# Optimization experiments

Hardware: AMD Instinct MI355X
Metric: run time of the kernel (lower is better)

## Reference

```python
import jax, jax.numpy as jnp
import numpy as np

N, F_IN, F_OUT = 8192, 256, 128


def setup_inputs() -> dict:
    key = jax.random.key(0)
    k1, k2, k3, k4 = jax.random.split(key, 4)
    h = jax.random.normal(k1, (N, F_IN), dtype=jnp.float32)
    adj = jax.random.randint(k2, (N, N), 0, 2, dtype=jnp.int32)
    # xavier-uniform-like init scales
    w_lim = float(np.sqrt(6.0 / (F_IN + F_OUT)))
    a_lim = float(np.sqrt(6.0 / (2 * F_OUT + 1)))
    W = jax.random.uniform(k3, (F_IN, F_OUT), jnp.float32, -w_lim, w_lim)
    a = jax.random.uniform(k4, (2 * F_OUT, 1), jnp.float32, -a_lim, a_lim)
    return {"h": h, "adj": adj, "W": W, "a": a}


def reference(h, adj, W, a):
    # Wh: [N, F_OUT]
    Wh = h @ W
    # Fused form of the pairwise-concat score: e[i,j] = leakyrelu(Wh_i.a1 + Wh_j.a2)
    a1 = a[:F_OUT]   # [F_OUT, 1]
    a2 = a[F_OUT:]   # [F_OUT, 1]
    s1 = Wh @ a1     # [N, 1]
    s2 = Wh @ a2     # [N, 1]
    e = jax.nn.leaky_relu(s1 + s2.T, negative_slope=0.2)  # [N, N]
    e = jnp.where(adj > 0, e, jnp.float32(-9e15))
    attention = jax.nn.softmax(e, axis=1)
    return attention @ Wh  # [N, F_OUT]
```

## Files before the change

kernel.cpp:

```cpp
#include <hip/hip_runtime.h>

#define N_   8192
#define FIN  256
#define FOUT 128

typedef _Float16 f16x8 __attribute__((ext_vector_type(8)));
typedef _Float16 f16x4 __attribute__((ext_vector_type(4)));
typedef float    f32x4 __attribute__((ext_vector_type(4)));

__global__ __launch_bounds__(256) void k_wh(
    const float* __restrict__ h, const float* __restrict__ W,
    const float* __restrict__ a, float* __restrict__ Wh,
    float* __restrict__ s1, float* __restrict__ s2)
{
    __shared__ float hrow[2][FIN];
    __shared__ float rbuf[2][2][2];
    const int t   = threadIdx.x;
    const int rh  = t >> 7;
    const int c   = t & 127;
    const int row = (blockIdx.x << 1) + rh;

    hrow[rh][c]       = h[(size_t)row * FIN + c];
    hrow[rh][c + 128] = h[(size_t)row * FIN + c + 128];
    __syncthreads();

    float acc = 0.f;
    #pragma unroll 8
    for (int k = 0; k < FIN; ++k)
        acc = fmaf(hrow[rh][k], W[k * FOUT + c], acc);

    Wh[(size_t)row * FOUT + c] = acc;

    float p1 = acc * a[c];
    float p2 = acc * a[FOUT + c];
    #pragma unroll
    for (int off = 32; off; off >>= 1) {
        p1 += __shfl_down(p1, off, 64);
        p2 += __shfl_down(p2, off, 64);
    }
    if ((t & 63) == 0) { rbuf[rh][c >> 6][0] = p1; rbuf[rh][c >> 6][1] = p2; }
    __syncthreads();
    if (c == 0) {
        s1[row] = rbuf[rh][0][0] + rbuf[rh][1][0];
        s2[row] = rbuf[rh][0][1] + rbuf[rh][1][1];
    }
}

__global__ __launch_bounds__(256) void k_tr(
    const float* __restrict__ Wh, _Float16* __restrict__ WhT)
{
    __shared__ float tile[64][129];
    const int t = threadIdx.x;
    const int rbase = blockIdx.x * 64;

    #pragma unroll
    for (int q = 0; q < 8; ++q) {
        int i4 = q * 256 + t;
        int r  = i4 >> 5;
        int c4 = (i4 & 31) * 4;
        *(float4*)&tile[r][c4] = *(const float4*)&Wh[(size_t)(rbase + r) * FOUT + c4];
    }
    __syncthreads();

    const int c = t >> 1, half = t & 1;
    _Float16 buf[32];
    #pragma unroll
    for (int r = 0; r < 32; ++r) buf[r] = (_Float16)tile[32 * half + r][c];
    #pragma unroll
    for (int q = 0; q < 4; ++q)
        *(f16x8*)&WhT[(size_t)c * N_ + rbase + 32 * half + 8 * q] = *(f16x8*)&buf[8 * q];
}

__global__ __launch_bounds__(512, 4) void k_attn(
    const int* __restrict__ adj, const _Float16* __restrict__ WhT,
    const float* __restrict__ s1g, const float* __restrict__ s2g,
    float* __restrict__ num_g, float* __restrict__ den_g)
{
    __shared__ _Float16 pA[32 * 64];

    const int t  = threadIdx.x;
    const int w  = t >> 6;
    const int l  = t & 63;

    const int rb    = blockIdx.x & 255;
    const int sp    = blockIdx.x >> 8;
    const int rbase = rb * 32;
    const int jbase = sp * 2048;
    const int NT    = 2048 / 64;

    const int r  = t >> 4;
    const int j0 = (t & 15) << 2;
    const float s1r = s1g[rbase + r];
    const int* __restrict__ adjrow = adj + (size_t)(rbase + r) * N_;

    const int ln15 = l & 15, lq = l >> 4;
    const _Float16* __restrict__ bptr =
        WhT + (size_t)(16 * w + ln15) * N_ + 8 * lq;
    const int a_row0 = ln15;
    const int a_row1 = 16 + ln15;
    const int a_sw0  = (a_row0 & 7) << 3;
    const int a_sw1  = (a_row1 & 7) << 3;

    f32x4 acc0 = {0.f, 0.f, 0.f, 0.f};
    f32x4 acc1 = {0.f, 0.f, 0.f, 0.f};
    float denp = 0.f;

    int4   av  = *(const int4*)(adjrow + jbase + j0);
    float4 s2v = *(const float4*)(s2g + jbase + j0);

    for (int tile = 0; tile < NT; ++tile) {
        const int jb = jbase + tile * 64;

        float e, p0, p1, p2, p3;
        e = s1r + s2v.x; e = e > 0.f ? e : 0.2f * e; p0 = av.x ? __expf(e - 4.f) : 0.f;
        e = s1r + s2v.y; e = e > 0.f ? e : 0.2f * e; p1 = av.y ? __expf(e - 4.f) : 0.f;
        e = s1r + s2v.z; e = e > 0.f ? e : 0.2f * e; p2 = av.z ? __expf(e - 4.f) : 0.f;
        e = s1r + s2v.w; e = e > 0.f ? e : 0.2f * e; p3 = av.w ? __expf(e - 4.f) : 0.f;
        _Float16 h0 = (_Float16)p0, h1 = (_Float16)p1,
                 h2 = (_Float16)p2, h3 = (_Float16)p3;
        denp += (float)h0 + (float)h1 + (float)h2 + (float)h3;
        f16x4 pv = {h0, h1, h2, h3};
        *(f16x4*)(pA + r * 64 + (j0 ^ ((r & 7) << 3))) = pv;

        __syncthreads();

        const int jn = (tile + 1 < NT) ? jb + 64 : jbase;
        int4   av_n  = *(const int4*)(adjrow + jn + j0);
        float4 s2v_n = *(const float4*)(s2g + jn + j0);

        f16x8 b0 = *(const f16x8*)(bptr + jb);
        f16x8 b1 = *(const f16x8*)(bptr + jb + 32);

        f16x8 a00 = *(const f16x8*)(pA + a_row0 * 64 + ((8 * lq)      ^ a_sw0));
        f16x8 a01 = *(const f16x8*)(pA + a_row0 * 64 + ((32 + 8 * lq) ^ a_sw0));
        f16x8 a10 = *(const f16x8*)(pA + a_row1 * 64 + ((8 * lq)      ^ a_sw1));
        f16x8 a11 = *(const f16x8*)(pA + a_row1 * 64 + ((32 + 8 * lq) ^ a_sw1));

        acc0 = __builtin_amdgcn_mfma_f32_16x16x32_f16(a00, b0, acc0, 0, 0, 0);
        acc0 = __builtin_amdgcn_mfma_f32_16x16x32_f16(a01, b1, acc0, 0, 0, 0);
        acc1 = __builtin_amdgcn_mfma_f32_16x16x32_f16(a10, b0, acc1, 0, 0, 0);
        acc1 = __builtin_amdgcn_mfma_f32_16x16x32_f16(a11, b1, acc1, 0, 0, 0);

        __syncthreads();
        av = av_n; s2v = s2v_n;
    }

    denp += __shfl_xor(denp, 1, 64);
    denp += __shfl_xor(denp, 2, 64);
    denp += __shfl_xor(denp, 4, 64);
    denp += __shfl_xor(denp, 8, 64);
    if ((t & 15) == 0)
        den_g[(size_t)sp * N_ + rbase + r] = denp;

    const int colg = 16 * w + ln15;
    const int rq   = lq * 4;
    #pragma unroll
    for (int q = 0; q < 4; ++q) {
        num_g[((size_t)sp * N_ + rbase + rq + q)      * FOUT + colg] = acc0[q];
        num_g[((size_t)sp * N_ + rbase + 16 + rq + q) * FOUT + colg] = acc1[q];
    }
}

__global__ __launch_bounds__(256) void k_norm(
    const float* __restrict__ num_g, const float* __restrict__ den_g,
    float* __restrict__ out)
{
    const int idx4 = blockIdx.x * 256 + threadIdx.x;
    const int i  = idx4 >> 5;
    const int c4 = (idx4 & 31) * 4;

    float4 s = {0.f, 0.f, 0.f, 0.f};
    float  d = 0.f;
    #pragma unroll
    for (int sp = 0; sp < 4; ++sp) {
        float4 v = *(const float4*)(num_g + ((size_t)sp * N_ + i) * FOUT + c4);
        s.x += v.x; s.y += v.y; s.z += v.z; s.w += v.w;
        d += den_g[(size_t)sp * N_ + i];
    }
    const float inv = 1.f / d;
    float4 o = {s.x * inv, s.y * inv, s.z * inv, s.w * inv};
    *(float4*)&out[(size_t)i * FOUT + c4] = o;
}

extern "C" void kernel_launch(void* const* d_in, const int* in_sizes, int n_in,
                              void* d_out, int out_size, void* d_ws, size_t ws_size,
                              hipStream_t stream) {
    const float* h   = (const float*)d_in[0];
    const int*   adj = (const int*)d_in[1];
    const float* W   = (const float*)d_in[2];
    const float* a   = (const float*)d_in[3];
    float* out = (float*)d_out;

    char* ws = (char*)d_ws;
    float*    Wh  = (float*)ws;
    _Float16* WhT = (_Float16*)(ws + (4u << 20));
    float*    s1  = (float*)(ws + (6u << 20));
    float*    s2  = (float*)(ws + (6u << 20) + 32768);
    float*    num = (float*)(ws + (7u << 20));
    float*    den = (float*)(ws + (23u << 20));

    k_wh  <<<N_ / 2, 256, 0, stream>>>(h, W, a, Wh, s1, s2);
    k_tr  <<<N_ / 64, 256, 0, stream>>>(Wh, WhT);
    k_attn<<<1024, 512, 0, stream>>>(adj, WhT, s1, s2, num, den);
    k_norm<<<1024, 256, 0, stream>>>(num, den, out);
}
```

Baseline: 145.4 us.

## Double-buffer attention P tile with 128-wide K steps and LDS-staged s2

```diff
diff --git a/kernel.cpp b/kernel.cpp
--- a/kernel.cpp
+++ b/kernel.cpp
@@ -76,7 +76,8 @@
     const float* __restrict__ s1g, const float* __restrict__ s2g,
     float* __restrict__ num_g, float* __restrict__ den_g)
 {
-    __shared__ _Float16 pA[32 * 64];
+    __shared__ _Float16 pA[2][32][136];
+    __shared__ float s2s[2048];
 
     const int t  = threadIdx.x;
     const int w  = t >> 6;
@@ -86,64 +87,89 @@
     const int sp    = blockIdx.x >> 8;
     const int rbase = rb * 32;
     const int jbase = sp * 2048;
-    const int NT    = 2048 / 64;
+
+    *(float4*)&s2s[t * 4] = *(const float4*)&s2g[jbase + t * 4];
 
     const int r  = t >> 4;
-    const int j0 = (t & 15) << 2;
+    const int j0 = (t & 15) << 3;
     const float s1r = s1g[rbase + r];
-    const int* __restrict__ adjrow = adj + (size_t)(rbase + r) * N_;
+    const int* __restrict__ arow = adj + (size_t)(rbase + r) * N_ + jbase;
 
     const int ln15 = l & 15, lq = l >> 4;
     const _Float16* __restrict__ bptr =
-        WhT + (size_t)(16 * w + ln15) * N_ + 8 * lq;
-    const int a_row0 = ln15;
-    const int a_row1 = 16 + ln15;
-    const int a_sw0  = (a_row0 & 7) << 3;
-    const int a_sw1  = (a_row1 & 7) << 3;
+        WhT + (size_t)(16 * w + ln15) * N_ + jbase + 8 * lq;
 
     f32x4 acc0 = {0.f, 0.f, 0.f, 0.f};
     f32x4 acc1 = {0.f, 0.f, 0.f, 0.f};
     float denp = 0.f;
 
-    int4   av  = *(const int4*)(adjrow + jbase + j0);
-    float4 s2v = *(const float4*)(s2g + jbase + j0);
-
-    for (int tile = 0; tile < NT; ++tile) {
-        const int jb = jbase + tile * 64;
-
-        float e, p0, p1, p2, p3;
-        e = s1r + s2v.x; e = e > 0.f ? e : 0.2f * e; p0 = av.x ? __expf(e - 4.f) : 0.f;
-        e = s1r + s2v.y; e = e > 0.f ? e : 0.2f * e; p1 = av.y ? __expf(e - 4.f) : 0.f;
-        e = s1r + s2v.z; e = e > 0.f ? e : 0.2f * e; p2 = av.z ? __expf(e - 4.f) : 0.f;
-        e = s1r + s2v.w; e = e > 0.f ? e : 0.2f * e; p3 = av.w ? __expf(e - 4.f) : 0.f;
-        _Float16 h0 = (_Float16)p0, h1 = (_Float16)p1,
-                 h2 = (_Float16)p2, h3 = (_Float16)p3;
-        denp += (float)h0 + (float)h1 + (float)h2 + (float)h3;
-        f16x4 pv = {h0, h1, h2, h3};
-        *(f16x4*)(pA + r * 64 + (j0 ^ ((r & 7) << 3))) = pv;
-
-        __syncthreads();
-
-        const int jn = (tile + 1 < NT) ? jb + 64 : jbase;
-        int4   av_n  = *(const int4*)(adjrow + jn + j0);
-        float4 s2v_n = *(const float4*)(s2g + jn + j0);
-
+    auto computeP = [&](const int4& aA, const int4& aB, int tile, int buf) {
+        const float* s2p = &s2s[tile * 128 + j0];
+        float4 sA = *(const float4*)(s2p);
+        float4 sB = *(const float4*)(s2p + 4);
+        float m, e;
+        f16x8 pv;
+        m = s1r + sA.x; e = fmaxf(m, 0.2f * m); pv[0] = (_Float16)(aA.x ? __expf(e - 4.f) : 0.f);
+        m = s1r + sA.y; e = fmaxf(m, 0.2f * m); pv[1] = (_Float16)(aA.y ? __expf(e - 4.f) : 0.f);
+        m = s1r + sA.z; e = fmaxf(m, 0.2f * m); pv[2] = (_Float16)(aA.z ? __expf(e - 4.f) : 0.f);
+        m = s1r + sA.w; e = fmaxf(m, 0.2f * m); pv[3] = (_Float16)(aA.w ? __expf(e - 4.f) : 0.f);
+        m = s1r + sB.x; e = fmaxf(m, 0.2f * m); pv[4] = (_Float16)(aB.x ? __expf(e - 4.f) : 0.f);
+        m = s1r + sB.y; e = fmaxf(m, 0.2f * m); pv[5] = (_Float16)(aB.y ? __expf(e - 4.f) : 0.f);
+        m = s1r + sB.z; e = fmaxf(m, 0.2f * m); pv[6] = (_Float16)(aB.z ? __expf(e - 4.f) : 0.f);
+        m = s1r + sB.w; e = fmaxf(m, 0.2f * m); pv[7] = (_Float16)(aB.w ? __expf(e - 4.f) : 0.f);
+        denp += (float)pv[0] + (float)pv[1] + (float)pv[2] + (float)pv[3]
+              + (float)pv[4] + (float)pv[5] + (float)pv[6] + (float)pv[7];
+        *(f16x8*)&pA[buf][r][j0] = pv;
+    };
+
+    auto mmaTile = [&](int buf, int jb) {
         f16x8 b0 = *(const f16x8*)(bptr + jb);
         f16x8 b1 = *(const f16x8*)(bptr + jb + 32);
-
-        f16x8 a00 = *(const f16x8*)(pA + a_row0 * 64 + ((8 * lq)      ^ a_sw0));
-        f16x8 a01 = *(const f16x8*)(pA + a_row0 * 64 + ((32 + 8 * lq) ^ a_sw0));
-        f16x8 a10 = *(const f16x8*)(pA + a_row1 * 64 + ((8 * lq)      ^ a_sw1));
-        f16x8 a11 = *(const f16x8*)(pA + a_row1 * 64 + ((32 + 8 * lq) ^ a_sw1));
-
-        acc0 = __builtin_amdgcn_mfma_f32_16x16x32_f16(a00, b0, acc0, 0, 0, 0);
-        acc0 = __builtin_amdgcn_mfma_f32_16x16x32_f16(a01, b1, acc0, 0, 0, 0);
-        acc1 = __builtin_amdgcn_mfma_f32_16x16x32_f16(a10, b0, acc1, 0, 0, 0);
-        acc1 = __builtin_amdgcn_mfma_f32_16x16x32_f16(a11, b1, acc1, 0, 0, 0);
-
-        __syncthreads();
-        av = av_n; s2v = s2v_n;
-    }
+        f16x8 b2 = *(const f16x8*)(bptr + jb + 64);
+        f16x8 b3 = *(const f16x8*)(bptr + jb + 96);
+        const _Float16* a0p = &pA[buf][ln15][8 * lq];
+        const _Float16* a1p = &pA[buf][16 + ln15][8 * lq];
+        acc0 = __builtin_amdgcn_mfma_f32_16x16x32_f16(*(const f16x8*)(a0p),      b0, acc0, 0, 0, 0);
+        acc1 = __builtin_amdgcn_mfma_f32_16x16x32_f16(*(const f16x8*)(a1p),      b0, acc1, 0, 0, 0);
+        acc0 = __builtin_amdgcn_mfma_f32_16x16x32_f16(*(const f16x8*)(a0p + 32), b1, acc0, 0, 0, 0);
+        acc1 = __builtin_amdgcn_mfma_f32_16x16x32_f16(*(const f16x8*)(a1p + 32), b1, acc1, 0, 0, 0);
+        acc0 = __builtin_amdgcn_mfma_f32_16x16x32_f16(*(const f16x8*)(a0p + 64), b2, acc0, 0, 0, 0);
+        acc1 = __builtin_amdgcn_mfma_f32_16x16x32_f16(*(const f16x8*)(a1p + 64), b2, acc1, 0, 0, 0);
+        acc0 = __builtin_amdgcn_mfma_f32_16x16x32_f16(*(const f16x8*)(a0p + 96), b3, acc0, 0, 0, 0);
+        acc1 = __builtin_amdgcn_mfma_f32_16x16x32_f16(*(const f16x8*)(a1p + 96), b3, acc1, 0, 0, 0);
+    };
+
+    int4 av0A = *(const int4*)(arow + j0);
+    int4 av0B = *(const int4*)(arow + j0 + 4);
+    int4 av1A = *(const int4*)(arow + 128 + j0);
+    int4 av1B = *(const int4*)(arow + 128 + j0 + 4);
+
+    __syncthreads();
+    computeP(av0A, av0B, 0, 0);
+    __syncthreads();
+
+    for (int tt = 0; tt < 14; tt += 2) {
+        {
+            const int tn = tt + 2;
+            av0A = *(const int4*)(arow + tn * 128 + j0);
+            av0B = *(const int4*)(arow + tn * 128 + j0 + 4);
+            mmaTile(0, tt * 128);
+            computeP(av1A, av1B, tt + 1, 1);
+            __syncthreads();
+        }
+        {
+            const int tn = tt + 3;
+            av1A = *(const int4*)(arow + tn * 128 + j0);
+            av1B = *(const int4*)(arow + tn * 128 + j0 + 4);
+            mmaTile(1, (tt + 1) * 128);
+            computeP(av0A, av0B, tt + 2, 0);
+            __syncthreads();
+        }
+    }
+    mmaTile(0, 14 * 128);
+    computeP(av1A, av1B, 15, 1);
+    __syncthreads();
+    mmaTile(1, 15 * 128);
 
     denp += __shfl_xor(denp, 1, 64);
     denp += __shfl_xor(denp, 2, 64);
```

Result: faster. 132.2 us (-9.0%).

## Restructure attention kernel to per-wave 16-row tiles with register-only MFMA pipeline

Applied to the files above, without the earlier changes.

```diff
diff --git a/kernel.cpp b/kernel.cpp
--- a/kernel.cpp
+++ b/kernel.cpp
@@ -5,8 +5,8 @@
 #define FOUT 128
 
 typedef _Float16 f16x8 __attribute__((ext_vector_type(8)));
-typedef _Float16 f16x4 __attribute__((ext_vector_type(4)));
 typedef float    f32x4 __attribute__((ext_vector_type(4)));
+typedef unsigned int uint;
 
 __global__ __launch_bounds__(256) void k_wh(
     const float* __restrict__ h, const float* __restrict__ W,
@@ -41,13 +41,14 @@
     if ((t & 63) == 0) { rbuf[rh][c >> 6][0] = p1; rbuf[rh][c >> 6][1] = p2; }
     __syncthreads();
     if (c == 0) {
-        s1[row] = rbuf[rh][0][0] + rbuf[rh][1][0];
-        s2[row] = rbuf[rh][0][1] + rbuf[rh][1][1];
+        const float k2 = 1.44269504088896f;
+        s1[row] = (rbuf[rh][0][0] + rbuf[rh][1][0]) * k2;
+        s2[row] = (rbuf[rh][0][1] + rbuf[rh][1][1]) * k2;
     }
 }
 
 __global__ __launch_bounds__(256) void k_tr(
-    const float* __restrict__ Wh, _Float16* __restrict__ WhT)
+    const float* __restrict__ Wh, _Float16* __restrict__ WhTt)
 {
     __shared__ float tile[64][129];
     const int t = threadIdx.x;
@@ -66,98 +67,112 @@
     _Float16 buf[32];
     #pragma unroll
     for (int r = 0; r < 32; ++r) buf[r] = (_Float16)tile[32 * half + r][c];
+    _Float16* dst = WhTt + (size_t)(rbase / 32 + half) * 4096 + c * 32;
     #pragma unroll
     for (int q = 0; q < 4; ++q)
-        *(f16x8*)&WhT[(size_t)c * N_ + rbase + 32 * half + 8 * q] = *(f16x8*)&buf[8 * q];
-}
-
-__global__ __launch_bounds__(512, 4) void k_attn(
-    const int* __restrict__ adj, const _Float16* __restrict__ WhT,
+        *(f16x8*)(dst + 8 * q) = *(f16x8*)&buf[8 * q];
+}
+
+__global__ __launch_bounds__(256) void k_attn(
+    const int* __restrict__ adj, const _Float16* __restrict__ WhTt,
     const float* __restrict__ s1g, const float* __restrict__ s2g,
     float* __restrict__ num_g, float* __restrict__ den_g)
 {
-    __shared__ _Float16 pA[32 * 64];
-
     const int t  = threadIdx.x;
     const int w  = t >> 6;
     const int l  = t & 63;
-
-    const int rb    = blockIdx.x & 255;
-    const int sp    = blockIdx.x >> 8;
-    const int rbase = rb * 32;
+    const int ln15 = l & 15, lq = l >> 4;
+
+    const int sp    = blockIdx.x >> 7;
+    const int rg    = (blockIdx.x & 127) * 4 + w;
+    const int rbase = rg * 16;
     const int jbase = sp * 2048;
-    const int NT    = 2048 / 64;
-
-    const int r  = t >> 4;
-    const int j0 = (t & 15) << 2;
-    const float s1r = s1g[rbase + r];
-    const int* __restrict__ adjrow = adj + (size_t)(rbase + r) * N_;
-
-    const int ln15 = l & 15, lq = l >> 4;
-    const _Float16* __restrict__ bptr =
-        WhT + (size_t)(16 * w + ln15) * N_ + 8 * lq;
-    const int a_row0 = ln15;
-    const int a_row1 = 16 + ln15;
-    const int a_sw0  = (a_row0 & 7) << 3;
-    const int a_sw1  = (a_row1 & 7) << 3;
-
-    f32x4 acc0 = {0.f, 0.f, 0.f, 0.f};
-    f32x4 acc1 = {0.f, 0.f, 0.f, 0.f};
+
+    const float s1r = s1g[rbase + ln15];
+    const int* __restrict__ arow =
+        adj + (size_t)(rbase + ln15) * N_ + jbase + 8 * lq;
+    const float* __restrict__ s2p = s2g + jbase + 8 * lq;
+    const _Float16* __restrict__ bp =
+        WhTt + (size_t)(jbase >> 5) * 4096 + ln15 * 32 + 8 * lq;
+
+    f32x4 acc[8];
+    #pragma unroll
+    for (int g = 0; g < 8; ++g) acc[g] = (f32x4){0.f, 0.f, 0.f, 0.f};
     float denp = 0.f;
 
-    int4   av  = *(const int4*)(adjrow + jbase + j0);
-    float4 s2v = *(const float4*)(s2g + jbase + j0);
-
-    for (int tile = 0; tile < NT; ++tile) {
-        const int jb = jbase + tile * 64;
-
-        float e, p0, p1, p2, p3;
-        e = s1r + s2v.x; e = e > 0.f ? e : 0.2f * e; p0 = av.x ? __expf(e - 4.f) : 0.f;
-        e = s1r + s2v.y; e = e > 0.f ? e : 0.2f * e; p1 = av.y ? __expf(e - 4.f) : 0.f;
-        e = s1r + s2v.z; e = e > 0.f ? e : 0.2f * e; p2 = av.z ? __expf(e - 4.f) : 0.f;
-        e = s1r + s2v.w; e = e > 0.f ? e : 0.2f * e; p3 = av.w ? __expf(e - 4.f) : 0.f;
-        _Float16 h0 = (_Float16)p0, h1 = (_Float16)p1,
-                 h2 = (_Float16)p2, h3 = (_Float16)p3;
-        denp += (float)h0 + (float)h1 + (float)h2 + (float)h3;
-        f16x4 pv = {h0, h1, h2, h3};
-        *(f16x4*)(pA + r * 64 + (j0 ^ ((r & 7) << 3))) = pv;
-
-        __syncthreads();
-
-        const int jn = (tile + 1 < NT) ? jb + 64 : jbase;
-        int4   av_n  = *(const int4*)(adjrow + jn + j0);
-        float4 s2v_n = *(const float4*)(s2g + jn + j0);
-
-        f16x8 b0 = *(const f16x8*)(bptr + jb);
-        f16x8 b1 = *(const f16x8*)(bptr + jb + 32);
-
-        f16x8 a00 = *(const f16x8*)(pA + a_row0 * 64 + ((8 * lq)      ^ a_sw0));
-        f16x8 a01 = *(const f16x8*)(pA + a_row0 * 64 + ((32 + 8 * lq) ^ a_sw0));
-        f16x8 a10 = *(const f16x8*)(pA + a_row1 * 64 + ((8 * lq)      ^ a_sw1));
-        f16x8 a11 = *(const f16x8*)(pA + a_row1 * 64 + ((32 + 8 * lq) ^ a_sw1));
-
-        acc0 = __builtin_amdgcn_mfma_f32_16x16x32_f16(a00, b0, acc0, 0, 0, 0);
-        acc0 = __builtin_amdgcn_mfma_f32_16x16x32_f16(a01, b1, acc0, 0, 0, 0);
-        acc1 = __builtin_amdgcn_mfma_f32_16x16x32_f16(a10, b0, acc1, 0, 0, 0);
-        acc1 = __builtin_amdgcn_mfma_f32_16x16x32_f16(a11, b1, acc1, 0, 0, 0);
-
-        __syncthreads();
-        av = av_n; s2v = s2v_n;
-    }
-
-    denp += __shfl_xor(denp, 1, 64);
-    denp += __shfl_xor(denp, 2, 64);
-    denp += __shfl_xor(denp, 4, 64);
-    denp += __shfl_xor(denp, 8, 64);
-    if ((t & 15) == 0)
-        den_g[(size_t)sp * N_ + rbase + r] = denp;
-
-    const int colg = 16 * w + ln15;
-    const int rq   = lq * 4;
-    #pragma unroll
-    for (int q = 0; q < 4; ++q) {
-        num_g[((size_t)sp * N_ + rbase + rq + q)      * FOUT + colg] = acc0[q];
-        num_g[((size_t)sp * N_ + rbase + 16 + rq + q) * FOUT + colg] = acc1[q];
+    auto LA = [&](int tile, int h) { return *(const int4*)(arow + tile * 32 + 4 * h); };
+    auto LS = [&](int tile, int h) { return *(const float4*)(s2p + tile * 32 + 4 * h); };
+
+    auto loadB = [&](f16x8* Bd, int tile) {
+        const _Float16* p = bp + (size_t)tile * 4096;
+        #pragma unroll
+        for (int g = 0; g < 8; ++g) Bd[g] = *(const f16x8*)(p + g * 512);
+    };
+
+    auto computeP = [&](const int4& a0, const int4& a1,
+                        const float4& sA, const float4& sB) -> f16x8 {
+        const float bias = -5.77078016f;
+        float m, e;
+        f16x8 pv;
+        m = s1r + sA.x; e = fmaxf(m, 0.2f * m); pv[0] = (_Float16)(a0.x ? __builtin_amdgcn_exp2f(e + bias) : 0.f);
+        m = s1r + sA.y; e = fmaxf(m, 0.2f * m); pv[1] = (_Float16)(a0.y ? __builtin_amdgcn_exp2f(e + bias) : 0.f);
+        m = s1r + sA.z; e = fmaxf(m, 0.2f * m); pv[2] = (_Float16)(a0.z ? __builtin_amdgcn_exp2f(e + bias) : 0.f);
+        m = s1r + sA.w; e = fmaxf(m, 0.2f * m); pv[3] = (_Float16)(a0.w ? __builtin_amdgcn_exp2f(e + bias) : 0.f);
+        m = s1r + sB.x; e = fmaxf(m, 0.2f * m); pv[4] = (_Float16)(a1.x ? __builtin_amdgcn_exp2f(e + bias) : 0.f);
+        m = s1r + sB.y; e = fmaxf(m, 0.2f * m); pv[5] = (_Float16)(a1.y ? __builtin_amdgcn_exp2f(e + bias) : 0.f);
+        m = s1r + sB.z; e = fmaxf(m, 0.2f * m); pv[6] = (_Float16)(a1.z ? __builtin_amdgcn_exp2f(e + bias) : 0.f);
+        m = s1r + sB.w; e = fmaxf(m, 0.2f * m); pv[7] = (_Float16)(a1.w ? __builtin_amdgcn_exp2f(e + bias) : 0.f);
+        denp += (float)pv[0] + (float)pv[1] + (float)pv[2] + (float)pv[3]
+              + (float)pv[4] + (float)pv[5] + (float)pv[6] + (float)pv[7];
+        return pv;
+    };
+
+    auto mmaAll = [&](const f16x8& af, const f16x8* B) {
+        __builtin_amdgcn_s_setprio(1);
+        #pragma unroll
+        for (int g = 0; g < 8; ++g)
+            acc[g] = __builtin_amdgcn_mfma_f32_16x16x32_f16(af, B[g], acc[g], 0, 0, 0);
+        __builtin_amdgcn_s_setprio(0);
+    };
+
+    int4   aA0 = LA(0, 0), aA1 = LA(0, 1);
+    int4   aB0 = LA(1, 0), aB1 = LA(1, 1);
+    float4 sA0 = LS(0, 0), sA1 = LS(0, 1);
+    float4 sB0, sB1;
+    f16x8  Bc[8], Bn[8];
+    loadB(Bc, 0);
+
+    for (int tt = 0; tt < 64; tt += 2) {
+        {
+            const int tn = (tt + 1 < 64) ? tt + 1 : 63;
+            sB0 = LS(tn, 0); sB1 = LS(tn, 1);
+            loadB(Bn, tn);
+            f16x8 af = computeP(aA0, aA1, sA0, sA1);
+            const int ta = (tt + 2 < 64) ? tt + 2 : 63;
+            aA0 = LA(ta, 0); aA1 = LA(ta, 1);
+            mmaAll(af, Bc);
+        }
+        {
+            const int tn = (tt + 2 < 64) ? tt + 2 : 63;
+            sA0 = LS(tn, 0); sA1 = LS(tn, 1);
+            loadB(Bc, tn);
+            f16x8 af = computeP(aB0, aB1, sB0, sB1);
+            const int ta = (tt + 3 < 64) ? tt + 3 : 63;
+            aB0 = LA(ta, 0); aB1 = LA(ta, 1);
+            mmaAll(af, Bn);
+        }
+    }
+
+    denp += __shfl_xor(denp, 16, 64);
+    denp += __shfl_xor(denp, 32, 64);
+    if (l < 16)
+        den_g[(size_t)sp * N_ + rbase + ln15] = denp;
+
+    #pragma unroll
+    for (int g = 0; g < 8; ++g) {
+        #pragma unroll
+        for (int e = 0; e < 4; ++e)
+            num_g[((size_t)sp * N_ + rbase + 4 * lq + e) * FOUT + 16 * g + ln15] = acc[g][e];
     }
 }
 
@@ -192,15 +207,15 @@
     float* out = (float*)d_out;
 
     char* ws = (char*)d_ws;
-    float*    Wh  = (float*)ws;
-    _Float16* WhT = (_Float16*)(ws + (4u << 20));
-    float*    s1  = (float*)(ws + (6u << 20));
-    float*    s2  = (float*)(ws + (6u << 20) + 32768);
-    float*    num = (float*)(ws + (7u << 20));
-    float*    den = (float*)(ws + (23u << 20));
+    float*    Wh   = (float*)ws;
+    _Float16* WhTt = (_Float16*)(ws + (4u << 20));
+    float*    s1   = (float*)(ws + (6u << 20));
+    float*    s2   = (float*)(ws + (6u << 20) + 32768);
+    float*    num  = (float*)(ws + (7u << 20));
+    float*    den  = (float*)(ws + (23u << 20));
 
     k_wh  <<<N_ / 2, 256, 0, stream>>>(h, W, a, Wh, s1, s2);
-    k_tr  <<<N_ / 64, 256, 0, stream>>>(Wh, WhT);
-    k_attn<<<1024, 512, 0, stream>>>(adj, WhT, s1, s2, num, den);
-    k_norm<<<1024, 256, 0, stream>>>(num, den, out);
-}
+    k_tr  <<<N_ / 64, 256, 0, stream>>>(Wh, WhTt);
+    k_attn<<<512,   256, 0, stream>>>(adj, WhTt, s1, s2, num, den);
+    k_norm<<<1024,  256, 0, stream>>>(num, den, out);
+}
```

Result: slower. 163.5 us (+12.5%).
